# Kernel optimization log

Hardware: AMD Instinct MI355X
Metric: run time of the kernel (lower is better)

The kernel has to match this reference:

```python
import jax, jax.numpy as jnp
import numpy as np

NUM_BINS_X = 1024
NUM_BINS_Y = 1024
XL, XH, YL, YH = 0.0, 1024.0, 0.0, 1024.0
NUM_NODES = 4_000_000
NUM_FILLER = 1_000_000
NUM_PHYS = NUM_NODES - NUM_FILLER      # physical = movable + fixed
NUM_MOVABLE = 2_500_000
UNIT_PIN_CAPACITY = 2.0                # pins per unit area capacity
PIN_STRETCH_RATIO = 1.414              # DREAMPlace default sqrt(2)
MAX_ADJ = 2.5
MIN_ADJ = 1.0 / MAX_ADJ
SPAN = 4                               # max bins any box spans per axis (sizes <= 2*bin)


def setup_inputs() -> dict:
    key = jax.random.key(0)
    k1, k2, k3, k4, k5 = jax.random.split(key, 5)
    node_size_x = 0.5 + 1.5 * jax.random.uniform(k1, (NUM_NODES,), jnp.float32)
    node_size_y = 0.5 + 1.5 * jax.random.uniform(k2, (NUM_NODES,), jnp.float32)
    pos_x = XL + jax.random.uniform(k3, (NUM_NODES,), jnp.float32) * (XH - XL - 2.0)
    pos_y = YL + jax.random.uniform(k4, (NUM_NODES,), jnp.float32) * (YH - YL - 2.0)
    pos = jnp.concatenate([pos_x, pos_y])  # [2*num_nodes], x then y
    pin_weights = jax.random.randint(k5, (NUM_PHYS,), 1, 9, jnp.int32)
    return {"pos": pos, "node_size_x": node_size_x, "node_size_y": node_size_y,
            "pin_weights": pin_weights}


def _overlap(lo, hi, bin_lo, bin_size):
    # overlap length of interval [lo,hi] with bin [bin_lo, bin_lo+bin_size]
    return jnp.clip(jnp.minimum(hi, bin_lo + bin_size) - jnp.maximum(lo, bin_lo), 0.0, None)


def reference(pos, node_size_x, node_size_y, pin_weights):
    bsx = (XH - XL) / NUM_BINS_X
    bsy = (YH - YL) / NUM_BINS_Y
    dtype = pos.dtype

    # ---- phase 1: pin density map over stretched boxes of physical nodes ----
    sx = node_size_x[:NUM_PHYS]
    sy = node_size_y[:NUM_PHYS]
    hx = 0.5 * jnp.maximum(bsx * PIN_STRETCH_RATIO, sx)  # half stretched extent
    hy = 0.5 * jnp.maximum(bsy * PIN_STRETCH_RATIO, sy)
    cx = pos[:NUM_PHYS] + 0.5 * sx
    cy = pos[NUM_NODES:NUM_NODES + NUM_PHYS] + 0.5 * sy
    xmin, xmax = cx - hx, cx + hx
    ymin, ymax = cy - hy, cy + hy
    dens = pin_weights.astype(dtype) / (4.0 * hx * hy)   # pins per unit area

    bxl = jnp.clip(jnp.floor((xmin - XL) / bsx).astype(jnp.int32), 0, NUM_BINS_X - 1)
    byl = jnp.clip(jnp.floor((ymin - YL) / bsy).astype(jnp.int32), 0, NUM_BINS_Y - 1)

    pmap = jnp.zeros(NUM_BINS_X * NUM_BINS_Y, dtype)
    for di in range(SPAN):
        bx = bxl + di
        ox = _overlap(xmin, xmax, XL + bx.astype(dtype) * bsx, bsx)
        vx = bx < NUM_BINS_X
        for dj in range(SPAN):
            by = byl + dj
            oy = _overlap(ymin, ymax, YL + by.astype(dtype) * bsy, bsy)
            v = vx & (by < NUM_BINS_Y)
            idx = jnp.where(v, bx * NUM_BINS_Y + by, 0)
            val = jnp.where(v, dens * ox * oy, 0.0)
            pmap = pmap.at[idx].add(val)

    # density -> utilization: scatter added pins*overlap/area, divide by bin area
    pmap = pmap / (bsx * bsy)
    adj = jnp.clip(pmap / UNIT_PIN_CAPACITY, MIN_ADJ, MAX_ADJ)

    # ---- phase 2: per-movable-node pin-optimized area over actual footprint ----
    mx = pos[:NUM_MOVABLE]
    my = pos[NUM_NODES:NUM_NODES + NUM_MOVABLE]
    msx = node_size_x[:NUM_MOVABLE]
    msy = node_size_y[:NUM_MOVABLE]
    bxl2 = jnp.clip(jnp.floor((mx - XL) / bsx).astype(jnp.int32), 0, NUM_BINS_X - 1)
    byl2 = jnp.clip(jnp.floor((my - YL) / bsy).astype(jnp.int32), 0, NUM_BINS_Y - 1)

    area = jnp.zeros(NUM_MOVABLE, dtype)
    for di in range(SPAN):
        bx = bxl2 + di
        ox = _overlap(mx, mx + msx, XL + bx.astype(dtype) * bsx, bsx)
        vx = bx < NUM_BINS_X
        for dj in range(SPAN):
            by = byl2 + dj
            oy = _overlap(my, my + msy, YL + by.astype(dtype) * bsy, bsy)
            v = vx & (by < NUM_BINS_Y)
            idx = jnp.where(v, bx * NUM_BINS_Y + by, 0)
            area = area + jnp.where(v, ox * oy * adj[idx], 0.0)
    return area
```

## Files before the change

### kernel.cpp

```cpp
#include <hip/hip_runtime.h>

#define NBX 1024
#define NBY 1024
#define TS 64
#define NTX (NBX / TS)
#define NTY (NBY / TS)
#define NTILES (NTX * NTY)
#define LW 66
#define LSTRIDE 67
#define CAP 13056
#define CAPM 11008

#define FB_BLOCK 512
#define FB_K 8
#define FB_CHUNK (FB_BLOCK * FB_K)

#define PMAP_SCALE 131072.0f
#define PMAP_INV   (1.0f / 131072.0f)

static constexpr int NUM_NODES   = 4000000;
static constexpr int NUM_PHYS    = 3000000;
static constexpr int NUM_MOVABLE = 2500000;
static constexpr int HALF_MOV    = NUM_MOVABLE / 2;

typedef unsigned long long u64;

static constexpr size_t OFF_PMAP  = 0;
static constexpr size_t OFF_CURS  = OFF_PMAP + (size_t)NBX * NBY * 4;
static constexpr size_t OFF_CURSM = OFF_CURS + NTILES * 4;
static constexpr size_t OFF_SLAB  = ((OFF_CURSM + NTILES * 4 + 15) / 16) * 16;
static constexpr size_t OFF_MSLAB = ((OFF_SLAB + (size_t)NTILES * CAP * 8 + 15) / 16) * 16;
static constexpr size_t WS_FULL   = OFF_MSLAB + (size_t)NTILES * CAPM * 12;

__global__ void __launch_bounds__(FB_BLOCK)
fill_both(const float* __restrict__ pos, const float* __restrict__ nsx,
          const float* __restrict__ nsy, const int* __restrict__ pw,
          unsigned* __restrict__ curs, unsigned* __restrict__ cursm,
          uint2* __restrict__ slab, uint3* __restrict__ mslab) {
    __shared__ unsigned cntp[NTILES], cntm[NTILES];
    __shared__ unsigned basep[NTILES], basem[NTILES];
    const int tid = threadIdx.x;
    const int b0  = blockIdx.x * FB_CHUNK;

    if (tid < NTILES) { cntp[tid] = 0u; cntm[tid] = 0u; }
    __syncthreads();

    u64 P[FB_K];
    u64 M[FB_K];
    int TPM[FB_K];

    #pragma unroll
    for (int k = 0; k < FB_K; ++k) {
        int i = b0 + k * FB_BLOCK + tid;
        int tp = -1, tm = -1;
        if (i < NUM_PHYS) {
            float mx = pos[i], my = pos[NUM_NODES + i];
            float sx = nsx[i], sy = nsy[i];
            float hx = 0.5f * fmaxf(1.414f, sx);
            float hy = 0.5f * fmaxf(1.414f, sy);
            unsigned qhx = (unsigned)__float2int_rn((hx - 0.7f) * 1024.0f);
            unsigned qhy = (unsigned)__float2int_rn((hy - 0.7f) * 1024.0f);
            float hxd = 0.7f + (float)qhx * (1.0f / 1024.0f);
            float hyd = 0.7f + (float)qhy * (1.0f / 1024.0f);
            float xmin = mx + 0.5f * sx - hxd;
            float ymin = my + 0.5f * sy - hyd;
            int bxl = min(max((int)floorf(xmin), 0), NBX - 1);
            int byl = min(max((int)floorf(ymin), 0), NBY - 1);
            tp = (bxl >> 6) * NTY + (byl >> 6);
            int bx0 = (tp >> 4) << 6, by0 = (tp & 15) << 6;
            unsigned ex = (unsigned)__float2int_rn((xmin - (float)bx0 + 1.0f) * 8192.0f);
            unsigned ey = (unsigned)__float2int_rn((ymin - (float)by0 + 1.0f) * 8192.0f);
            P[k] = (u64)ex | ((u64)ey << 20) | ((u64)qhx << 40)
                 | ((u64)qhy << 50) | ((u64)(unsigned)(pw[i] - 1) << 60);
            atomicAdd(&cntp[tp], 1u);
            if (i < NUM_MOVABLE) {
                int bxm = min(max((int)floorf(mx), 0), NBX - 1);
                int bym = min(max((int)floorf(my), 0), NBY - 1);
                tm = (bxm >> 6) * NTY + (bym >> 6);
                int bx0m = (tm >> 4) << 6, by0m = (tm & 15) << 6;
                unsigned exm = (unsigned)__float2int_rn((mx - (float)bx0m) * 8192.0f);
                unsigned eym = (unsigned)__float2int_rn((my - (float)by0m) * 8192.0f);
                unsigned qsx = (unsigned)__float2int_rn((sx - 0.5f) * 2048.0f);
                unsigned qsy = (unsigned)__float2int_rn((sy - 0.5f) * 2048.0f);
                M[k] = (u64)exm | ((u64)eym << 20) | ((u64)qsx << 40) | ((u64)qsy << 52);
                atomicAdd(&cntm[tm], 1u);
            }
        }
        TPM[k] = (tp & 0xffff) | (tm << 16);
    }
    __syncthreads();

    if (tid < NTILES) {
        unsigned np = cntp[tid];
        basep[tid] = np ? atomicAdd(&curs[tid], np) : 0u;
        unsigned nm = cntm[tid];
        basem[tid] = nm ? atomicAdd(&cursm[tid], nm) : 0u;
        cntp[tid] = 0u; cntm[tid] = 0u;
    }
    __syncthreads();

    #pragma unroll
    for (int k = 0; k < FB_K; ++k) {
        int tp = (int)(short)(TPM[k] & 0xffff);
        int tm = TPM[k] >> 16;
        if (tp >= 0) {
            unsigned p = basep[tp] + atomicAdd(&cntp[tp], 1u);
            if (p < CAP)
                slab[(size_t)tp * CAP + p] =
                    make_uint2((unsigned)P[k], (unsigned)(P[k] >> 32));
        }
        if (tm >= 0) {
            int i = b0 + k * FB_BLOCK + tid;
            unsigned p = basem[tm] + atomicAdd(&cntm[tm], 1u);
            if (p < CAPM)
                mslab[(size_t)tm * CAPM + p] =
                    make_uint3((unsigned)M[k], (unsigned)(M[k] >> 32), (unsigned)i);
        }
    }
}

__global__ void __launch_bounds__(1024)
tile_scatter(const uint2* __restrict__ slab, const unsigned* __restrict__ curs,
             float* __restrict__ pmap) {
    __shared__ unsigned lds[LW * LSTRIDE];
    int t  = blockIdx.x;
    int bx0 = (t >> 4) << 6, by0 = (t & 15) << 6;

    for (int c = threadIdx.x; c < LW * LSTRIDE; c += 1024) lds[c] = 0u;
    __syncthreads();

    unsigned n = min(curs[t], (unsigned)CAP);
    const uint2* sl = slab + (size_t)t * CAP;

    unsigned k = threadIdx.x;
    uint2 p = (k < n) ? sl[k] : make_uint2(0u, 0u);
    while (k < n) {
        unsigned kn = k + 1024;
        uint2 pn = (kn < n) ? sl[kn] : make_uint2(0u, 0u);

        u64 P = (u64)p.x | ((u64)p.y << 32);
        float xminl = (float)(P & 0xFFFFFu)         * (1.0f / 8192.0f) - 1.0f;
        float yminl = (float)((P >> 20) & 0xFFFFFu) * (1.0f / 8192.0f) - 1.0f;
        float hx = 0.7f + (float)((P >> 40) & 0x3FFu) * (1.0f / 1024.0f);
        float hy = 0.7f + (float)((P >> 50) & 0x3FFu) * (1.0f / 1024.0f);
        float pwv  = (float)(1u + (unsigned)(P >> 60));
        float dens = pwv / (4.0f * hx * hy);
        float xmaxl = xminl + 2.0f * hx;
        float ymaxl = yminl + 2.0f * hy;

        int lx0 = min(max((int)floorf(xminl), 0), TS - 1);
        int ly0 = min(max((int)floorf(yminl), 0), TS - 1);
        #pragma unroll
        for (int di = 0; di < 3; ++di) {
            float bl = (float)(lx0 + di);
            float ox = fminf(xmaxl, bl + 1.0f) - fmaxf(xminl, bl);
            if (ox <= 0.0f) continue;
            float dox = dens * ox;
            #pragma unroll
            for (int dj = 0; dj < 3; ++dj) {
                float bly = (float)(ly0 + dj);
                float oy  = fminf(ymaxl, bly + 1.0f) - fmaxf(yminl, bly);
                if (oy > 0.0f) {
                    unsigned q = (unsigned)__float2int_rn(dox * oy * PMAP_SCALE);
                    atomicAdd(&lds[(lx0 + di) * LSTRIDE + (ly0 + dj)], q);
                }
            }
        }
        p = pn;
        k = kn;
    }
    __syncthreads();

    for (int c = threadIdx.x; c < LW * LW; c += 1024) {
        int lx = c / LW, ly = c - lx * LW;
        int bx = bx0 + lx, by = by0 + ly;
        if (bx >= NBX || by >= NBY) continue;
        float v = (float)lds[lx * LSTRIDE + ly] * PMAP_INV;
        bool interior = (lx >= 2) & (lx < TS) & (ly >= 2) & (ly < TS);
        if (interior)
            pmap[bx * NBY + by] = v;
        else if (v != 0.0f)
            atomicAdd(&pmap[bx * NBY + by], v);
    }
}

__global__ void __launch_bounds__(1024)
gather_tile(const uint3* __restrict__ mslab, const unsigned* __restrict__ cursm,
            const float* __restrict__ pmap, float* __restrict__ out) {
    __shared__ float adj[LW * LSTRIDE];
    int t  = blockIdx.x;
    int bx0 = (t >> 4) << 6, by0 = (t & 15) << 6;

    for (int c = threadIdx.x; c < LW * LW; c += 1024) {
        int r = c / LW, col = c - r * LW;
        int bx = min(bx0 + r,  NBX - 1);
        int by = min(by0 + col, NBY - 1);
        adj[r * LSTRIDE + col] =
            fminf(fmaxf(pmap[bx * NBY + by] * 0.5f, 0.4f), 2.5f);
    }
    __syncthreads();

    unsigned n = min(cursm[t], (unsigned)CAPM);
    const uint3* sl = mslab + (size_t)t * CAPM;

    for (unsigned k = threadIdx.x; k < n; k += 1024) {
        uint3 p = sl[k];
        u64 M = (u64)p.x | ((u64)p.y << 32);
        float mxl = (float)(M & 0xFFFFFu)         * (1.0f / 8192.0f);
        float myl = (float)((M >> 20) & 0xFFFFFu) * (1.0f / 8192.0f);
        float sx  = 0.5f + (float)((M >> 40) & 0xFFFu) * (1.0f / 2048.0f);
        float sy  = 0.5f + (float)(M >> 52)            * (1.0f / 2048.0f);
        float xmaxl = mxl + sx;
        float ymaxl = myl + sy;

        int lx0 = min((int)mxl, TS - 1);
        int ly0 = min((int)myl, TS - 1);

        float area = 0.0f;
        #pragma unroll
        for (int di = 0; di < 3; ++di) {
            float bl = (float)(lx0 + di);
            float ox = fmaxf(fminf(xmaxl, bl + 1.0f) - fmaxf(mxl, bl), 0.0f);
            #pragma unroll
            for (int dj = 0; dj < 3; ++dj) {
                float bly = (float)(ly0 + dj);
                float oy  = fmaxf(fminf(ymaxl, bly + 1.0f) - fmaxf(myl, bly), 0.0f);
                area += ox * oy * adj[(lx0 + di) * LSTRIDE + (ly0 + dj)];
            }
        }
        out[p.z] = area;
    }
}

__global__ void __launch_bounds__(256)
scatter_pin(const float* __restrict__ pos, const float* __restrict__ nsx,
            const float* __restrict__ nsy, const int* __restrict__ pw,
            float* __restrict__ pmap) {
    int i = blockIdx.x * blockDim.x + threadIdx.x;
    if (i >= NUM_PHYS) return;
    float sx = nsx[i], sy = nsy[i];
    float hx = 0.5f * fmaxf(1.414f, sx);
    float hy = 0.5f * fmaxf(1.414f, sy);
    float cx = pos[i] + 0.5f * sx;
    float cy = pos[NUM_NODES + i] + 0.5f * sy;
    float xmin = cx - hx, xmax = cx + hx;
    float ymin = cy - hy, ymax = cy + hy;
    float dens = (float)pw[i] / (4.0f * hx * hy);
    int bxl = min(max((int)floorf(xmin), 0), NBX - 1);
    int byl = min(max((int)floorf(ymin), 0), NBY - 1);
    #pragma unroll
    for (int di = 0; di < 3; ++di) {
        float bl = (float)(bxl + di);
        float ox = fminf(xmax, bl + 1.0f) - fmaxf(xmin, bl);
        if (ox <= 0.0f) continue;
        float dox = dens * ox;
        int base = min(bxl + di, NBX - 1) * NBY;
        #pragma unroll
        for (int dj = 0; dj < 3; ++dj) {
            float bly = (float)(byl + dj);
            float oy  = fminf(ymax, bly + 1.0f) - fmaxf(ymin, bly);
            if (oy > 0.0f) atomicAdd(&pmap[base + min(byl + dj, NBY - 1)], dox * oy);
        }
    }
}

__device__ __forceinline__ float gather_one(const float* __restrict__ pos,
                                            const float* __restrict__ nsx,
                                            const float* __restrict__ nsy,
                                            const float* __restrict__ pmap,
                                            int i) {
    float mx = pos[i];
    float my = pos[NUM_NODES + i];
    float xmax = mx + nsx[i];
    float ymax = my + nsy[i];
    int bxl = min(max((int)floorf(mx), 0), NBX - 1);
    int byl = min(max((int)floorf(my), 0), NBY - 1);
    float ox[3], oy[3];
    int rowb[3], colb[3];
    #pragma unroll
    for (int d = 0; d < 3; ++d) {
        float bl  = (float)(bxl + d);
        float bly = (float)(byl + d);
        ox[d] = fmaxf(fminf(xmax, bl + 1.0f) - fmaxf(mx, bl), 0.0f);
        oy[d] = fmaxf(fminf(ymax, bly + 1.0f) - fmaxf(my, bly), 0.0f);
        rowb[d] = min(bxl + d, NBX - 1) * NBY;
        colb[d] = min(byl + d, NBY - 1);
    }
    float area = 0.0f;
    #pragma unroll
    for (int di = 0; di < 3; ++di)
        #pragma unroll
        for (int dj = 0; dj < 3; ++dj) {
            float a = fminf(fmaxf(pmap[rowb[di] + colb[dj]] * 0.5f, 0.4f), 2.5f);
            area += ox[di] * oy[dj] * a;
        }
    return area;
}

__global__ void __launch_bounds__(256)
gather_area(const float* __restrict__ pos, const float* __restrict__ nsx,
            const float* __restrict__ nsy, const float* __restrict__ pmap,
            float* __restrict__ out) {
    int i = blockIdx.x * blockDim.x + threadIdx.x;
    if (i >= HALF_MOV) return;
    int i2 = i + HALF_MOV;
    float a1 = gather_one(pos, nsx, nsy, pmap, i);
    float a2 = gather_one(pos, nsx, nsy, pmap, i2);
    out[i]  = a1;
    out[i2] = a2;
}

extern "C" void kernel_launch(void* const* d_in, const int* in_sizes, int n_in,
                              void* d_out, int out_size, void* d_ws, size_t ws_size,
                              hipStream_t stream) {
    const float* pos = (const float*)d_in[0];
    const float* nsx = (const float*)d_in[1];
    const float* nsy = (const float*)d_in[2];
    const int*   pw  = (const int*)d_in[3];
    float* out = (float*)d_out;

    char* ws = (char*)d_ws;
    float*    pmap  = (float*)(ws + OFF_PMAP);
    unsigned* curs  = (unsigned*)(ws + OFF_CURS);
    unsigned* cursm = (unsigned*)(ws + OFF_CURSM);
    uint2*    slab  = (uint2*)(ws + OFF_SLAB);
    uint3*    mslab = (uint3*)(ws + OFF_MSLAB);

    if (ws_size >= WS_FULL) {
        hipMemsetAsync(ws, 0, OFF_SLAB, stream);
        int grid = (NUM_PHYS + FB_CHUNK - 1) / FB_CHUNK;
        fill_both   <<<grid, FB_BLOCK, 0, stream>>>(pos, nsx, nsy, pw,
                                                    curs, cursm, slab, mslab);
        tile_scatter<<<NTILES, 1024, 0, stream>>>(slab, curs, pmap);
        gather_tile <<<NTILES, 1024, 0, stream>>>(mslab, cursm, pmap, out);
    } else {
        hipMemsetAsync(pmap, 0, (size_t)NBX * NBY * sizeof(float), stream);
        scatter_pin <<<(NUM_PHYS + 255) / 256, 256, 0, stream>>>(pos, nsx, nsy, pw, pmap);
        gather_area <<<(HALF_MOV + 255) / 256, 256, 0, stream>>>(pos, nsx, nsy, pmap, out);
    }
}
```

Measured before the change: 188.4 us.

## Stage binned records in LDS sorted by tile for coalesced slab writes

The fill kernel now keeps each element's rank from the first-pass shared atomic and computes a block-wide prefix scan of the per-tile counts. Records are placed into shared-memory staging arrays in tile order, then written to the global slabs with consecutive threads covering consecutive slots of each tile. This replaces scattered per-element global stores, and the second round of shared atomics, with mostly contiguous runs. The cost is about 53 KB of extra LDS per block, which may reduce occupancy, plus several more barriers.

```diff
diff --git a/kernel.cpp b/kernel.cpp
--- a/kernel.cpp
+++ b/kernel.cpp
@@ -38,7 +38,12 @@
           unsigned* __restrict__ curs, unsigned* __restrict__ cursm,
           uint2* __restrict__ slab, uint3* __restrict__ mslab) {
     __shared__ unsigned cntp[NTILES], cntm[NTILES];
+    __shared__ unsigned offp[NTILES], offm[NTILES];
     __shared__ unsigned basep[NTILES], basem[NTILES];
+    __shared__ unsigned wsum[8];
+    __shared__ unsigned SA[FB_CHUNK], SB[FB_CHUNK], SC[FB_CHUNK];
+    __shared__ unsigned char ST[FB_CHUNK];
+
     const int tid = threadIdx.x;
     const int b0  = blockIdx.x * FB_CHUNK;
 
@@ -48,6 +53,7 @@
     u64 P[FB_K];
     u64 M[FB_K];
     int TPM[FB_K];
+    unsigned rkP[FB_K], rkM[FB_K];
 
     #pragma unroll
     for (int k = 0; k < FB_K; ++k) {
@@ -72,7 +78,7 @@
             unsigned ey = (unsigned)__float2int_rn((ymin - (float)by0 + 1.0f) * 8192.0f);
             P[k] = (u64)ex | ((u64)ey << 20) | ((u64)qhx << 40)
                  | ((u64)qhy << 50) | ((u64)(unsigned)(pw[i] - 1) << 60);
-            atomicAdd(&cntp[tp], 1u);
+            rkP[k] = atomicAdd(&cntp[tp], 1u);
             if (i < NUM_MOVABLE) {
                 int bxm = min(max((int)floorf(mx), 0), NBX - 1);
                 int bym = min(max((int)floorf(my), 0), NBY - 1);
@@ -83,38 +89,83 @@
                 unsigned qsx = (unsigned)__float2int_rn((sx - 0.5f) * 2048.0f);
                 unsigned qsy = (unsigned)__float2int_rn((sy - 0.5f) * 2048.0f);
                 M[k] = (u64)exm | ((u64)eym << 20) | ((u64)qsx << 40) | ((u64)qsy << 52);
-                atomicAdd(&cntm[tm], 1u);
+                rkM[k] = atomicAdd(&cntm[tm], 1u);
             }
         }
         TPM[k] = (tp & 0xffff) | (tm << 16);
     }
     __syncthreads();
 
-    if (tid < NTILES) {
-        unsigned np = cntp[tid];
-        basep[tid] = np ? atomicAdd(&curs[tid], np) : 0u;
-        unsigned nm = cntm[tid];
-        basem[tid] = nm ? atomicAdd(&cursm[tid], nm) : 0u;
-        cntp[tid] = 0u; cntm[tid] = 0u;
+    {
+        const int lane   = tid & 63;
+        const int scanId = tid & 255;
+        const bool isMov = tid >= 256;
+        unsigned* cnt = isMov ? cntm : cntp;
+        unsigned* off = isMov ? offm : offp;
+        unsigned* bs  = isMov ? basem : basep;
+        unsigned* gc  = isMov ? cursm : curs;
+
+        unsigned v = cnt[scanId];
+        unsigned x = v;
+        #pragma unroll
+        for (int d = 1; d < 64; d <<= 1) {
+            unsigned y = __shfl_up(x, d);
+            if (lane >= d) x += y;
+        }
+        if (lane == 63) wsum[tid >> 6] = x;
+        __syncthreads();
+        unsigned add = 0;
+        const int w0  = isMov ? 4 : 0;
+        const int myw = scanId >> 6;
+        for (int w = 0; w < myw; ++w) add += wsum[w0 + w];
+        off[scanId] = x + add - v;
+        bs[scanId]  = v ? atomicAdd(&gc[scanId], v) : 0u;
     }
     __syncthreads();
 
     #pragma unroll
     for (int k = 0; k < FB_K; ++k) {
         int tp = (int)(short)(TPM[k] & 0xffff);
+        if (tp >= 0) {
+            unsigned s = offp[tp] + rkP[k];
+            SA[s] = (unsigned)P[k];
+            SB[s] = (unsigned)(P[k] >> 32);
+            ST[s] = (unsigned char)tp;
+        }
+    }
+    __syncthreads();
+
+    {
+        unsigned totP = offp[NTILES - 1] + cntp[NTILES - 1];
+        for (unsigned j = tid; j < totP; j += FB_BLOCK) {
+            unsigned tile = ST[j];
+            unsigned p = basep[tile] + (j - offp[tile]);
+            if (p < CAP)
+                slab[(size_t)tile * CAP + p] = make_uint2(SA[j], SB[j]);
+        }
+    }
+    __syncthreads();
+
+    #pragma unroll
+    for (int k = 0; k < FB_K; ++k) {
         int tm = TPM[k] >> 16;
-        if (tp >= 0) {
-            unsigned p = basep[tp] + atomicAdd(&cntp[tp], 1u);
-            if (p < CAP)
-                slab[(size_t)tp * CAP + p] =
-                    make_uint2((unsigned)P[k], (unsigned)(P[k] >> 32));
-        }
         if (tm >= 0) {
-            int i = b0 + k * FB_BLOCK + tid;
-            unsigned p = basem[tm] + atomicAdd(&cntm[tm], 1u);
+            unsigned s = offm[tm] + rkM[k];
+            SA[s] = (unsigned)M[k];
+            SB[s] = (unsigned)(M[k] >> 32);
+            SC[s] = (unsigned)(b0 + k * FB_BLOCK + tid);
+            ST[s] = (unsigned char)tm;
+        }
+    }
+    __syncthreads();
+
+    {
+        unsigned totM = offm[NTILES - 1] + cntm[NTILES - 1];
+        for (unsigned j = tid; j < totM; j += FB_BLOCK) {
+            unsigned tile = ST[j];
+            unsigned p = basem[tile] + (j - offm[tile]);
             if (p < CAPM)
-                mslab[(size_t)tm * CAPM + p] =
-                    make_uint3((unsigned)M[k], (unsigned)(M[k] >> 32), (unsigned)i);
+                mslab[(size_t)tile * CAPM + p] = make_uint3(SA[j], SB[j], SC[j]);
         }
     }
 }
```

After: 183.2 us. 2.8% less time.

## Coalesce binning writes via local sort, split scatter tiles, drop movable slab

Applied to the files above, without the earlier changes.

The fill kernel now only bins physical nodes. Each block computes a prefix sum of its per-tile counts and stages records in shared memory sorted by tile, so global slab writes come out contiguous per tile instead of scattered. The movable-node binning and the tile-based gather are removed, and area is computed with the direct global pmap gather. tile_scatter is split over two blocks per tile for more parallelism, which means every output bin is now written with atomics instead of plain stores.

```diff
diff --git a/kernel.cpp b/kernel.cpp
--- a/kernel.cpp
+++ b/kernel.cpp
@@ -9,11 +9,12 @@
 #define LW 66
 #define LSTRIDE 67
 #define CAP 13056
-#define CAPM 11008
 
 #define FB_BLOCK 512
 #define FB_K 8
 #define FB_CHUNK (FB_BLOCK * FB_K)
+
+#define SPLIT 2
 
 #define PMAP_SCALE 131072.0f
 #define PMAP_INV   (1.0f / 131072.0f)
@@ -27,32 +28,34 @@
 
 static constexpr size_t OFF_PMAP  = 0;
 static constexpr size_t OFF_CURS  = OFF_PMAP + (size_t)NBX * NBY * 4;
-static constexpr size_t OFF_CURSM = OFF_CURS + NTILES * 4;
-static constexpr size_t OFF_SLAB  = ((OFF_CURSM + NTILES * 4 + 15) / 16) * 16;
-static constexpr size_t OFF_MSLAB = ((OFF_SLAB + (size_t)NTILES * CAP * 8 + 15) / 16) * 16;
-static constexpr size_t WS_FULL   = OFF_MSLAB + (size_t)NTILES * CAPM * 12;
+static constexpr size_t OFF_SLAB  = ((OFF_CURS + NTILES * 4 + 15) / 16) * 16;
+static constexpr size_t WS_FULL   = OFF_SLAB + (size_t)NTILES * CAP * 8;
 
 __global__ void __launch_bounds__(FB_BLOCK)
-fill_both(const float* __restrict__ pos, const float* __restrict__ nsx,
+fill_phys(const float* __restrict__ pos, const float* __restrict__ nsx,
           const float* __restrict__ nsy, const int* __restrict__ pw,
-          unsigned* __restrict__ curs, unsigned* __restrict__ cursm,
-          uint2* __restrict__ slab, uint3* __restrict__ mslab) {
-    __shared__ unsigned cntp[NTILES], cntm[NTILES];
-    __shared__ unsigned basep[NTILES], basem[NTILES];
+          unsigned* __restrict__ curs, uint2* __restrict__ slab) {
+    __shared__ unsigned cnt[NTILES];
+    __shared__ unsigned off[NTILES];
+    __shared__ unsigned D[NTILES];
+    __shared__ unsigned wsum[4];
+    __shared__ uint2 SAB[FB_CHUNK];
+    __shared__ unsigned short ST[FB_CHUNK];
+
     const int tid = threadIdx.x;
     const int b0  = blockIdx.x * FB_CHUNK;
 
-    if (tid < NTILES) { cntp[tid] = 0u; cntm[tid] = 0u; }
+    if (tid < NTILES) cnt[tid] = 0u;
     __syncthreads();
 
     u64 P[FB_K];
-    u64 M[FB_K];
-    int TPM[FB_K];
+    int TP[FB_K];
+    unsigned rk[FB_K];
 
     #pragma unroll
     for (int k = 0; k < FB_K; ++k) {
         int i = b0 + k * FB_BLOCK + tid;
-        int tp = -1, tm = -1;
+        int tp = -1;
         if (i < NUM_PHYS) {
             float mx = pos[i], my = pos[NUM_NODES + i];
             float sx = nsx[i], sy = nsy[i];
@@ -72,49 +75,54 @@
             unsigned ey = (unsigned)__float2int_rn((ymin - (float)by0 + 1.0f) * 8192.0f);
             P[k] = (u64)ex | ((u64)ey << 20) | ((u64)qhx << 40)
                  | ((u64)qhy << 50) | ((u64)(unsigned)(pw[i] - 1) << 60);
-            atomicAdd(&cntp[tp], 1u);
-            if (i < NUM_MOVABLE) {
-                int bxm = min(max((int)floorf(mx), 0), NBX - 1);
-                int bym = min(max((int)floorf(my), 0), NBY - 1);
-                tm = (bxm >> 6) * NTY + (bym >> 6);
-                int bx0m = (tm >> 4) << 6, by0m = (tm & 15) << 6;
-                unsigned exm = (unsigned)__float2int_rn((mx - (float)bx0m) * 8192.0f);
-                unsigned eym = (unsigned)__float2int_rn((my - (float)by0m) * 8192.0f);
-                unsigned qsx = (unsigned)__float2int_rn((sx - 0.5f) * 2048.0f);
-                unsigned qsy = (unsigned)__float2int_rn((sy - 0.5f) * 2048.0f);
-                M[k] = (u64)exm | ((u64)eym << 20) | ((u64)qsx << 40) | ((u64)qsy << 52);
-                atomicAdd(&cntm[tm], 1u);
+            rk[k] = atomicAdd(&cnt[tp], 1u);
+        }
+        TP[k] = tp;
+    }
+    __syncthreads();
+
+    {
+        const int lane = tid & 63;
+        unsigned v = 0, x = 0;
+        if (tid < NTILES) {
+            v = cnt[tid];
+            x = v;
+            #pragma unroll
+            for (int d = 1; d < 64; d <<= 1) {
+                unsigned y = __shfl_up(x, d);
+                if (lane >= d) x += y;
             }
-        }
-        TPM[k] = (tp & 0xffff) | (tm << 16);
-    }
-    __syncthreads();
-
-    if (tid < NTILES) {
-        unsigned np = cntp[tid];
-        basep[tid] = np ? atomicAdd(&curs[tid], np) : 0u;
-        unsigned nm = cntm[tid];
-        basem[tid] = nm ? atomicAdd(&cursm[tid], nm) : 0u;
-        cntp[tid] = 0u; cntm[tid] = 0u;
+            if (lane == 63) wsum[tid >> 6] = x;
+        }
+        __syncthreads();
+        if (tid < NTILES) {
+            unsigned add = 0;
+            for (int w = 0; w < (tid >> 6); ++w) add += wsum[w];
+            unsigned o = x + add - v;
+            unsigned base = v ? atomicAdd(&curs[tid], v) : 0u;
+            off[tid] = o;
+            D[tid]   = base - o;
+        }
     }
     __syncthreads();
 
     #pragma unroll
     for (int k = 0; k < FB_K; ++k) {
-        int tp = (int)(short)(TPM[k] & 0xffff);
-        int tm = TPM[k] >> 16;
-        if (tp >= 0) {
-            unsigned p = basep[tp] + atomicAdd(&cntp[tp], 1u);
+        if (TP[k] >= 0) {
+            unsigned s = off[TP[k]] + rk[k];
+            SAB[s] = make_uint2((unsigned)P[k], (unsigned)(P[k] >> 32));
+            ST[s]  = (unsigned short)TP[k];
+        }
+    }
+    __syncthreads();
+
+    {
+        unsigned tot = off[NTILES - 1] + cnt[NTILES - 1];
+        for (unsigned j = tid; j < tot; j += FB_BLOCK) {
+            unsigned tile = ST[j];
+            unsigned p = D[tile] + j;
             if (p < CAP)
-                slab[(size_t)tp * CAP + p] =
-                    make_uint2((unsigned)P[k], (unsigned)(P[k] >> 32));
-        }
-        if (tm >= 0) {
-            int i = b0 + k * FB_BLOCK + tid;
-            unsigned p = basem[tm] + atomicAdd(&cntm[tm], 1u);
-            if (p < CAPM)
-                mslab[(size_t)tm * CAPM + p] =
-                    make_uint3((unsigned)M[k], (unsigned)(M[k] >> 32), (unsigned)i);
+                slab[(size_t)tile * CAP + p] = SAB[j];
         }
     }
 }
@@ -123,7 +131,8 @@
 tile_scatter(const uint2* __restrict__ slab, const unsigned* __restrict__ curs,
              float* __restrict__ pmap) {
     __shared__ unsigned lds[LW * LSTRIDE];
-    int t  = blockIdx.x;
+    int t   = blockIdx.x / SPLIT;
+    int sub = blockIdx.x - t * SPLIT;
     int bx0 = (t >> 4) << 6, by0 = (t & 15) << 6;
 
     for (int c = threadIdx.x; c < LW * LSTRIDE; c += 1024) lds[c] = 0u;
@@ -132,10 +141,10 @@
     unsigned n = min(curs[t], (unsigned)CAP);
     const uint2* sl = slab + (size_t)t * CAP;
 
-    unsigned k = threadIdx.x;
+    unsigned k = threadIdx.x + sub * 1024;
     uint2 p = (k < n) ? sl[k] : make_uint2(0u, 0u);
     while (k < n) {
-        unsigned kn = k + 1024;
+        unsigned kn = k + SPLIT * 1024;
         uint2 pn = (kn < n) ? sl[kn] : make_uint2(0u, 0u);
 
         u64 P = (u64)p.x | ((u64)p.y << 32);
@@ -176,60 +185,55 @@
         int bx = bx0 + lx, by = by0 + ly;
         if (bx >= NBX || by >= NBY) continue;
         float v = (float)lds[lx * LSTRIDE + ly] * PMAP_INV;
-        bool interior = (lx >= 2) & (lx < TS) & (ly >= 2) & (ly < TS);
-        if (interior)
-            pmap[bx * NBY + by] = v;
-        else if (v != 0.0f)
+        if (v != 0.0f)
             atomicAdd(&pmap[bx * NBY + by], v);
     }
 }
 
-__global__ void __launch_bounds__(1024)
-gather_tile(const uint3* __restrict__ mslab, const unsigned* __restrict__ cursm,
-            const float* __restrict__ pmap, float* __restrict__ out) {
-    __shared__ float adj[LW * LSTRIDE];
-    int t  = blockIdx.x;
-    int bx0 = (t >> 4) << 6, by0 = (t & 15) << 6;
-
-    for (int c = threadIdx.x; c < LW * LW; c += 1024) {
-        int r = c / LW, col = c - r * LW;
-        int bx = min(bx0 + r,  NBX - 1);
-        int by = min(by0 + col, NBY - 1);
-        adj[r * LSTRIDE + col] =
-            fminf(fmaxf(pmap[bx * NBY + by] * 0.5f, 0.4f), 2.5f);
-    }
-    __syncthreads();
-
-    unsigned n = min(cursm[t], (unsigned)CAPM);
-    const uint3* sl = mslab + (size_t)t * CAPM;
-
-    for (unsigned k = threadIdx.x; k < n; k += 1024) {
-        uint3 p = sl[k];
-        u64 M = (u64)p.x | ((u64)p.y << 32);
-        float mxl = (float)(M & 0xFFFFFu)         * (1.0f / 8192.0f);
-        float myl = (float)((M >> 20) & 0xFFFFFu) * (1.0f / 8192.0f);
-        float sx  = 0.5f + (float)((M >> 40) & 0xFFFu) * (1.0f / 2048.0f);
-        float sy  = 0.5f + (float)(M >> 52)            * (1.0f / 2048.0f);
-        float xmaxl = mxl + sx;
-        float ymaxl = myl + sy;
-
-        int lx0 = min((int)mxl, TS - 1);
-        int ly0 = min((int)myl, TS - 1);
-
-        float area = 0.0f;
+__device__ __forceinline__ float gather_one(const float* __restrict__ pos,
+                                            const float* __restrict__ nsx,
+                                            const float* __restrict__ nsy,
+                                            const float* __restrict__ pmap,
+                                            int i) {
+    float mx = pos[i];
+    float my = pos[NUM_NODES + i];
+    float xmax = mx + nsx[i];
+    float ymax = my + nsy[i];
+    int bxl = min(max((int)floorf(mx), 0), NBX - 1);
+    int byl = min(max((int)floorf(my), 0), NBY - 1);
+    float ox[3], oy[3];
+    int rowb[3], colb[3];
+    #pragma unroll
+    for (int d = 0; d < 3; ++d) {
+        float bl  = (float)(bxl + d);
+        float bly = (float)(byl + d);
+        ox[d] = fmaxf(fminf(xmax, bl + 1.0f) - fmaxf(mx, bl), 0.0f);
+        oy[d] = fmaxf(fminf(ymax, bly + 1.0f) - fmaxf(my, bly), 0.0f);
+        rowb[d] = min(bxl + d, NBX - 1) * NBY;
+        colb[d] = min(byl + d, NBY - 1);
+    }
+    float area = 0.0f;
+    #pragma unroll
+    for (int di = 0; di < 3; ++di)
         #pragma unroll
-        for (int di = 0; di < 3; ++di) {
-            float bl = (float)(lx0 + di);
-            float ox = fmaxf(fminf(xmaxl, bl + 1.0f) - fmaxf(mxl, bl), 0.0f);
-            #pragma unroll
-            for (int dj = 0; dj < 3; ++dj) {
-                float bly = (float)(ly0 + dj);
-                float oy  = fmaxf(fminf(ymaxl, bly + 1.0f) - fmaxf(myl, bly), 0.0f);
-                area += ox * oy * adj[(lx0 + di) * LSTRIDE + (ly0 + dj)];
-            }
-        }
-        out[p.z] = area;
-    }
+        for (int dj = 0; dj < 3; ++dj) {
+            float a = fminf(fmaxf(pmap[rowb[di] + colb[dj]] * 0.5f, 0.4f), 2.5f);
+            area += ox[di] * oy[dj] * a;
+        }
+    return area;
+}
+
+__global__ void __launch_bounds__(256)
+gather_area(const float* __restrict__ pos, const float* __restrict__ nsx,
+            const float* __restrict__ nsy, const float* __restrict__ pmap,
+            float* __restrict__ out) {
+    int i = blockIdx.x * blockDim.x + threadIdx.x;
+    if (i >= HALF_MOV) return;
+    int i2 = i + HALF_MOV;
+    float a1 = gather_one(pos, nsx, nsy, pmap, i);
+    float a2 = gather_one(pos, nsx, nsy, pmap, i2);
+    out[i]  = a1;
+    out[i2] = a2;
 }
 
 __global__ void __launch_bounds__(256)
@@ -264,52 +268,6 @@
     }
 }
 
-__device__ __forceinline__ float gather_one(const float* __restrict__ pos,
-                                            const float* __restrict__ nsx,
-                                            const float* __restrict__ nsy,
-                                            const float* __restrict__ pmap,
-                                            int i) {
-    float mx = pos[i];
-    float my = pos[NUM_NODES + i];
-    float xmax = mx + nsx[i];
-    float ymax = my + nsy[i];
-    int bxl = min(max((int)floorf(mx), 0), NBX - 1);
-    int byl = min(max((int)floorf(my), 0), NBY - 1);
-    float ox[3], oy[3];
-    int rowb[3], colb[3];
-    #pragma unroll
-    for (int d = 0; d < 3; ++d) {
-        float bl  = (float)(bxl + d);
-        float bly = (float)(byl + d);
-        ox[d] = fmaxf(fminf(xmax, bl + 1.0f) - fmaxf(mx, bl), 0.0f);
-        oy[d] = fmaxf(fminf(ymax, bly + 1.0f) - fmaxf(my, bly), 0.0f);
-        rowb[d] = min(bxl + d, NBX - 1) * NBY;
-        colb[d] = min(byl + d, NBY - 1);
-    }
-    float area = 0.0f;
-    #pragma unroll
-    for (int di = 0; di < 3; ++di)
-        #pragma unroll
-        for (int dj = 0; dj < 3; ++dj) {
-            float a = fminf(fmaxf(pmap[rowb[di] + colb[dj]] * 0.5f, 0.4f), 2.5f);
-            area += ox[di] * oy[dj] * a;
-        }
-    return area;
-}
-
-__global__ void __launch_bounds__(256)
-gather_area(const float* __restrict__ pos, const float* __restrict__ nsx,
-            const float* __restrict__ nsy, const float* __restrict__ pmap,
-            float* __restrict__ out) {
-    int i = blockIdx.x * blockDim.x + threadIdx.x;
-    if (i >= HALF_MOV) return;
-    int i2 = i + HALF_MOV;
-    float a1 = gather_one(pos, nsx, nsy, pmap, i);
-    float a2 = gather_one(pos, nsx, nsy, pmap, i2);
-    out[i]  = a1;
-    out[i2] = a2;
-}
-
 extern "C" void kernel_launch(void* const* d_in, const int* in_sizes, int n_in,
                               void* d_out, int out_size, void* d_ws, size_t ws_size,
                               hipStream_t stream) {
@@ -322,17 +280,14 @@
     char* ws = (char*)d_ws;
     float*    pmap  = (float*)(ws + OFF_PMAP);
     unsigned* curs  = (unsigned*)(ws + OFF_CURS);
-    unsigned* cursm = (unsigned*)(ws + OFF_CURSM);
     uint2*    slab  = (uint2*)(ws + OFF_SLAB);
-    uint3*    mslab = (uint3*)(ws + OFF_MSLAB);
 
     if (ws_size >= WS_FULL) {
         hipMemsetAsync(ws, 0, OFF_SLAB, stream);
         int grid = (NUM_PHYS + FB_CHUNK - 1) / FB_CHUNK;
-        fill_both   <<<grid, FB_BLOCK, 0, stream>>>(pos, nsx, nsy, pw,
-                                                    curs, cursm, slab, mslab);
-        tile_scatter<<<NTILES, 1024, 0, stream>>>(slab, curs, pmap);
-        gather_tile <<<NTILES, 1024, 0, stream>>>(mslab, cursm, pmap, out);
+        fill_phys   <<<grid, FB_BLOCK, 0, stream>>>(pos, nsx, nsy, pw, curs, slab);
+        tile_scatter<<<NTILES * SPLIT, 1024, 0, stream>>>(slab, curs, pmap);
+        gather_area <<<(HALF_MOV + 255) / 256, 256, 0, stream>>>(pos, nsx, nsy, pmap, out);
     } else {
         hipMemsetAsync(pmap, 0, (size_t)NBX * NBY * sizeof(float), stream);
         scatter_pin <<<(NUM_PHYS + 255) / 256, 256, 0, stream>>>(pos, nsx, nsy, pw, pmap);
```

After: 212.0 us. 12.5% more time.
